# Optimization experiments

Measured on AMD Instinct MI355X. Metric: run time of the kernel, lower is better.

The kernel has to match this reference:

```python
import jax, jax.numpy as jnp
import numpy as np

B, S, H, R, K, L = 8, 2048, 512, 7, 10, 4
OFFSETS = np.array([-3, -2, -1, 1, 2, 3], dtype=np.int32)
BN_EPS = 1e-5


def setup_inputs() -> dict:
    key = jax.random.key(0)
    ks = jax.random.split(key, 12)
    u = lambda k, shape, s: jax.random.uniform(k, shape, minval=-s, maxval=s, dtype=jnp.float32)
    s3, sh, shr = 1.0 / np.sqrt(3.0), 1.0 / np.sqrt(H), 1.0 / np.sqrt(R * H)
    return {
        "n_coords": jax.random.normal(ks[0], (B, S, 3), jnp.float32),
        "ca_coords": jax.random.normal(ks[1], (B, S, 3), jnp.float32),
        "c_coords": jax.random.normal(ks[2], (B, S, 3), jnp.float32),
        "Wp": u(ks[3], (H, 3), s3),
        "bp": u(ks[4], (H,), s3),
        "Wlin": u(ks[5], (L, H, R * H), shr),
        "blin": u(ks[6], (L, H), shr),
        "Wself": u(ks[7], (L, H, H), sh),
        "bself": u(ks[8], (L, H), sh),
        "bn_gamma": jnp.ones((L, H), jnp.float32),
        "bn_beta": jnp.zeros((L, H), jnp.float32),
        "bn_mean": jax.random.normal(ks[9], (L, H), jnp.float32) * 0.1,
        "bn_var": jax.random.uniform(ks[10], (L, H), minval=0.5, maxval=1.5, dtype=jnp.float32),
    }


def _edges(pos):
    """Edge list per graph: sequential offsets -3..3 -> relations 0..5, KNN(k=10) -> relation 6."""
    i = jnp.arange(S)
    off = jnp.asarray(OFFSETS)
    dst_seq = i[:, None] + off[None, :]                            # [S,6]
    valid = (dst_seq >= 0) & (dst_seq < S)
    src_seq = jnp.broadcast_to(i[:, None], (S, 6))
    rel_seq = jnp.broadcast_to(jnp.arange(6, dtype=jnp.int32)[None, :], (S, 6))
    dst_seq = jnp.clip(dst_seq, 0, S - 1)
    # squared distances give the same topk-smallest ordering as torch.norm
    d2 = jnp.sum((pos[:, None, :] - pos[None, :, :]) ** 2, axis=-1)  # [S,S]
    _, knn = jax.lax.top_k(-d2, K + 1)                             # k+1 smallest, self first
    dst_knn = knn[:, 1:]                                           # drop self
    src_knn = jnp.broadcast_to(i[:, None], (S, K))
    rel_knn = jnp.full((S, K), 6, dtype=jnp.int32)
    src = jnp.concatenate([src_seq.reshape(-1), src_knn.reshape(-1)])
    dst = jnp.concatenate([dst_seq.reshape(-1), dst_knn.reshape(-1)])
    rel = jnp.concatenate([rel_seq.reshape(-1), rel_knn.reshape(-1)])
    w = jnp.concatenate([valid.reshape(-1).astype(pos.dtype),
                         jnp.ones((S * K,), pos.dtype)])
    return src, dst, rel, w


def _gearnet(ca_coords, Wp, bp, Wlin, blin, Wself, bself, bn_gamma, bn_beta, bn_mean, bn_var):
    def per_graph(pos):
        src, dst, rel, w = _edges(pos)
        seg = dst * R + rel                                        # node_out*num_relation + relation
        h = pos @ Wp.T + bp                                        # coord_projection: Linear(3, H)
        for l in range(L):
            msg = h[src] * w[:, None]                              # [E,H] gather + edge weight
            upd = jax.ops.segment_sum(msg, seg, num_segments=S * R)  # scatter-add per (node, relation)
            upd = upd.reshape(S, R * H)
            out = upd @ Wlin[l].T + blin[l] + h @ Wself[l].T + bself[l]
            out = (out - bn_mean[l]) * jax.lax.rsqrt(bn_var[l] + BN_EPS) * bn_gamma[l] + bn_beta[l]
            h = jax.nn.relu(out) + h                               # relu then short_cut residual
        return h
    return jax.vmap(per_graph)(ca_coords)                          # [B,S,H]


def reference(n_coords, ca_coords, c_coords, Wp, bp, Wlin, blin, Wself, bself,
              bn_gamma, bn_beta, bn_mean, bn_var):
    # n_coords / c_coords are accepted but unused, exactly as in the original forward.
    return _gearnet(ca_coords, Wp, bp, Wlin, blin, Wself, bself,
                    bn_gamma, bn_beta, bn_mean, bn_var)
```

## Files before the change

### kernel.cpp

```cpp
#include <hip/hip_runtime.h>
#include <stdint.h>

#define B_ 8
#define S_ 2048
#define H_ 512
#define R_ 7
#define K_ 10
#define L_ 4
#define KT_ 4096
#define RH_ 3584

typedef __attribute__((ext_vector_type(8))) short bf16x8;
typedef __attribute__((ext_vector_type(4))) float f32x4;
typedef __attribute__((ext_vector_type(4))) unsigned short u16x4;
typedef unsigned long long u64;

__device__ __forceinline__ unsigned short f2bf(float f){
  unsigned int u = __float_as_uint(f);
  u = (u + 0x7fffu + ((u >> 16) & 1u)) >> 16;
  return (unsigned short)u;
}

__device__ __forceinline__ float bf2f(unsigned short s){
  return __uint_as_float(((unsigned int)s) << 16);
}

__device__ __forceinline__ f32x4 bf4load(const unsigned short* p){
  u16x4 v = *(const u16x4*)p;
  f32x4 o;
#pragma unroll
  for (int e = 0; e < 4; e++) o[e] = bf2f(v[e]);
  return o;
}

__device__ __forceinline__ void gload16(const void* g, void* lds){
  __builtin_amdgcn_global_load_lds(
      (const __attribute__((address_space(1))) unsigned int*)g,
      (__attribute__((address_space(3))) unsigned int*)lds, 16, 0, 0);
}

__global__ __launch_bounds__(256) void knn_kernel(const float* __restrict__ pos,
                                                  int* __restrict__ knn){
  __shared__ float px[S_], py[S_], pz[S_];
  int b = blockIdx.y;
  const float* p = pos + (size_t)b * S_ * 3;
  for (int idx = threadIdx.x; idx < S_; idx += 256){
    px[idx] = p[idx*3+0]; py[idx] = p[idx*3+1]; pz[idx] = p[idx*3+2];
  }
  __syncthreads();
  int w = threadIdx.x >> 6, l = threadIdx.x & 63;
  int i = blockIdx.x * 4 + w;
  float xi = px[i], yi = py[i], zi = pz[i];
  u64 best[10];
#pragma unroll
  for (int q = 0; q < 10; q++) best[q] = ~0ull;
  for (int j = l; j < S_; j += 64){
    if (j == i) continue;
    float dx = __fsub_rn(xi, px[j]);
    float dy = __fsub_rn(yi, py[j]);
    float dz = __fsub_rn(zi, pz[j]);
    float d2 = __fadd_rn(__fadd_rn(__fmul_rn(dx,dx), __fmul_rn(dy,dy)), __fmul_rn(dz,dz));
    u64 key = ((u64)__float_as_uint(d2) << 32) | (unsigned)j;
    if (key < best[9]){
      best[9] = key;
#pragma unroll
      for (int q = 9; q > 0; --q){
        u64 a = best[q-1], c = best[q];
        u64 lo = a < c ? a : c, hi = a < c ? c : a;
        best[q-1] = lo; best[q] = hi;
      }
    }
  }
  int* out = knn + ((size_t)b * S_ + i) * K_;
#pragma unroll
  for (int t = 0; t < 10; t++){
    u64 cand = best[0];
    u64 m = cand;
#pragma unroll
    for (int o = 32; o; o >>= 1){
      u64 other = __shfl_xor(m, o);
      if (other < m) m = other;
    }
    if (cand == m){
#pragma unroll
      for (int q = 0; q < 9; q++) best[q] = best[q+1];
      best[9] = ~0ull;
    }
    if (l == 0) out[t] = (int)(unsigned)(m & 0xffffffffu);
  }
}

__global__ void count_kernel(const int* __restrict__ knn, int* __restrict__ counts){
  int idx = blockIdx.x * 256 + threadIdx.x;
  int b = idx / (S_ * K_);
  int d = knn[idx];
  atomicAdd(&counts[b * S_ + d], 1);
}

__global__ __launch_bounds__(256) void scan_kernel(const int* __restrict__ counts,
                                                   int* __restrict__ row_start,
                                                   int* __restrict__ cursor){
  __shared__ int lds[256];
  int b = blockIdx.x, t = threadIdx.x;
  int base = b * S_;
  int v[8]; int s = 0;
#pragma unroll
  for (int e = 0; e < 8; e++){ v[e] = s; s += counts[base + t*8 + e]; }
  lds[t] = s;
  __syncthreads();
  int total = s;
  for (int o = 1; o < 256; o <<= 1){
    int add = 0;
    if (t >= o) add = lds[t - o];
    __syncthreads();
    lds[t] += add;
    __syncthreads();
  }
  int ex = lds[t] - total;
  int rb = b * (S_ + 1);
#pragma unroll
  for (int e = 0; e < 8; e++){
    int val = ex + v[e];
    row_start[rb + t*8 + e] = val;
    cursor[base + t*8 + e] = val;
  }
  if (t == 255) row_start[rb + S_] = lds[255];
}

__global__ void fill_kernel(const int* __restrict__ knn, int* __restrict__ cursor,
                            int* __restrict__ col){
  int idx = blockIdx.x * 256 + threadIdx.x;
  int b = idx / (S_ * K_);
  int i = (idx / K_) % S_;
  int d = knn[idx];
  int p = atomicAdd(&cursor[b * S_ + d], 1);
  col[(size_t)b * S_ * K_ + p] = i;
}

__global__ void sort_kernel(const int* __restrict__ row_start, int* __restrict__ col){
  int idx = blockIdx.x * 256 + threadIdx.x;
  int b = idx / S_, d = idx % S_;
  int rs = row_start[b*(S_+1)+d], re = row_start[b*(S_+1)+d+1];
  int* c = col + (size_t)b * S_ * K_;
  for (int a = rs + 1; a < re; ++a){
    int vv = c[a]; int q = a - 1;
    while (q >= rs && c[q] > vv){ c[q+1] = c[q]; --q; }
    c[q+1] = vv;
  }
}

__global__ void prepw_kernel(const float* __restrict__ Wlin, const float* __restrict__ Wself,
                             unsigned short* __restrict__ Wt){
  size_t e = ((size_t)blockIdx.x * 256 + threadIdx.x) * 8;
  int k = (int)(e & 4095);
  int j = (int)((e >> 12) & 511);
  int l = (int)(e >> 21);
  const float* src = (k < RH_) ? Wlin + ((size_t)l * H_ + j) * RH_ + k
                               : Wself + ((size_t)l * H_ + j) * H_ + (k - RH_);
  union { unsigned short s[8]; uint4 u; } pk;
#pragma unroll
  for (int t = 0; t < 8; t++) pk.s[t] = f2bf(src[t]);
  *(uint4*)&Wt[e] = pk.u;
}

__global__ void prepa_kernel(const float* __restrict__ gam, const float* __restrict__ bet,
                             const float* __restrict__ mean, const float* __restrict__ var,
                             const float* __restrict__ blin, const float* __restrict__ bself,
                             float* __restrict__ scale, float* __restrict__ shift){
  int idx = blockIdx.x * 256 + threadIdx.x;
  float sc = gam[idx] * rsqrtf(var[idx] + 1e-5f);
  scale[idx] = sc;
  shift[idx] = bet[idx] + (blin[idx] + bself[idx] - mean[idx]) * sc;
}

__global__ void inith_kernel(const float* __restrict__ pos, const float* __restrict__ Wp,
                             const float* __restrict__ bp, float* __restrict__ h,
                             unsigned short* __restrict__ hb){
  int idx = blockIdx.x * 256 + threadIdx.x;
  int j = (idx & 127) * 4;
  int bs = idx >> 7;
  const float* p = pos + (size_t)bs * 3;
  float x = p[0], y = p[1], z = p[2];
  f32x4 o;
#pragma unroll
  for (int e = 0; e < 4; e++){
    const float* wr = Wp + (j + e) * 3;
    o[e] = x * wr[0] + y * wr[1] + z * wr[2] + bp[j + e];
  }
  *(f32x4*)&h[(size_t)bs * H_ + j] = o;
  unsigned int w0 = f2bf(o[0]) | ((unsigned)f2bf(o[1]) << 16);
  unsigned int w1 = f2bf(o[2]) | ((unsigned)f2bf(o[3]) << 16);
  uint2 u; u.x = w0; u.y = w1;
  *(uint2*)&hb[(size_t)bs * H_ + j] = u;
}

__global__ __launch_bounds__(128) void hknn_kernel(const unsigned short* __restrict__ hb,
                                                   const int* __restrict__ row_start,
                                                   const int* __restrict__ col,
                                                   unsigned short* __restrict__ hk){
  int bx = blockIdx.x;
  int d = (bx & 7) * 256 + (bx >> 3);
  int b = blockIdx.y;
  int j = threadIdx.x * 4;
  int rs = row_start[b * (S_ + 1) + d];
  int re = row_start[b * (S_ + 1) + d + 1];
  const int* cl = col + (size_t)b * S_ * K_;
  f32x4 acc = {0.f, 0.f, 0.f, 0.f};
  for (int e = rs; e < re; ++e){
    int i = cl[e];
    acc += bf4load(&hb[((size_t)b * S_ + i) * H_ + j]);
  }
  u16x4 v;
#pragma unroll
  for (int e = 0; e < 4; e++) v[e] = f2bf(acc[e]);
  *(u16x4*)&hk[((size_t)b * S_ + d) * H_ + j] = v;
}

__global__ __launch_bounds__(256) void gemmf_kernel(
    const unsigned short* __restrict__ hbin,
    const unsigned short* __restrict__ hkn,
    const unsigned short* __restrict__ Wt,
    float* __restrict__ h,
    unsigned short* __restrict__ hbout,
    const float* __restrict__ scale,
    const float* __restrict__ shift,
    const unsigned short* __restrict__ zbuf){
  __shared__ unsigned short As[4][128 * 32];
  __shared__ unsigned short Bs[4][128 * 32];
  int tid = threadIdx.x;
  int nwg = gridDim.x;
  int q = nwg >> 3;
  int wg = blockIdx.x;
  int swz = (wg & 7) * q + (wg >> 3);
  int my = swz >> 2;
  int nx = swz & 3;
  int l = tid & 63, w = tid >> 6;
  int wrow = (w >> 1) * 64, wcol = (w & 1) * 64;
  int aBase = my * 128;
  int bBase = nx * 128;
  f32x4 acc[4][4] = {};

  int row0 = tid >> 2;
  int kc = (tid & 3) ^ ((row0 >> 1) & 3);
  int gr0 = aBase + row0, gr1 = gr0 + 64;
  const unsigned short* Bb0 = Wt + (size_t)(bBase + row0) * KT_ + kc * 8;
  const unsigned short* Bb1 = Wt + (size_t)(bBase + row0 + 64) * KT_ + kc * 8;
  int dst0 = tid * 8, dst1 = (tid + 256) * 8;

  const unsigned short *sa0, *sa1, *sb0, *sb1;

#define SETSLICE(rs) do {                                                     \
    int _r = (rs);                                                            \
    const unsigned short *_a0, *_a1;                                          \
    if (_r < 6){                                                              \
      int _sh = (_r < 3) ? (3 - _r) : (2 - _r);          \
      int _s0 = gr0 + _sh, _s1 = gr1 + _sh;                                   \
      _a0 = (((unsigned)_s0 >> 11) == ((unsigned)gr0 >> 11)) ? hbin + (size_t)_s0 * H_ : zbuf; \
      _a1 = (((unsigned)_s1 >> 11) == ((unsigned)gr1 >> 11)) ? hbin + (size_t)_s1 * H_ : zbuf; \
    } else {                                                                  \
      const unsigned short* _bs = (_r == 6) ? hkn : hbin;                     \
      _a0 = _bs + (size_t)gr0 * H_; _a1 = _bs + (size_t)gr1 * H_;             \
    }                                                                         \
    sa0 = _a0 + kc * 8; sa1 = _a1 + kc * 8;                                   \
    sb0 = Bb0 + _r * 512; sb1 = Bb1 + _r * 512;                               \
  } while (0)

#define STAGE(sl, ksl) do { int _ko = (ksl) * 32;          \
    gload16(sa0 + _ko, &As[sl][dst0]);                     \
    gload16(sa1 + _ko, &As[sl][dst1]);                     \
    gload16(sb0 + _ko, &Bs[sl][dst0]);                     \
    gload16(sb1 + _ko, &Bs[sl][dst1]);                     \
  } while (0)

  SETSLICE(0);
  STAGE(0, 0); STAGE(1, 1); STAGE(2, 2);

  int kcr = l >> 4, lr = l & 15;
  int s = 0;
  for (int r = 0; r < 8; ++r){
#pragma unroll
    for (int ks = 0; ks < 16; ++ks){
      int s3 = s + 3; if (s3 >= 4) s3 -= 4;
      if (r < 7 || ks < 13){
        if (ks == 13) SETSLICE(r + 1);
        STAGE(s3, (ks + 3) & 15);
      }
      if (r < 7 || ks < 13)  asm volatile("s_waitcnt vmcnt(12)" ::: "memory");
      else if (ks == 13)     asm volatile("s_waitcnt vmcnt(8)" ::: "memory");
      else if (ks == 14)     asm volatile("s_waitcnt vmcnt(4)" ::: "memory");
      else                   asm volatile("s_waitcnt vmcnt(0)" ::: "memory");
      __builtin_amdgcn_s_barrier();
      asm volatile("" ::: "memory");

      const unsigned short* Abuf = As[s];
      const unsigned short* Bbuf = Bs[s];
      bf16x8 af[4], bf[4];
#pragma unroll
      for (int mi = 0; mi < 4; mi++){
        int row = wrow + mi * 16 + lr;
        int slot = kcr ^ ((row >> 1) & 3);
        af[mi] = *(const bf16x8*)&Abuf[row * 32 + slot * 8];
      }
#pragma unroll
      for (int ni = 0; ni < 4; ni++){
        int row = wcol + ni * 16 + lr;
        int slot = kcr ^ ((row >> 1) & 3);
        bf[ni] = *(const bf16x8*)&Bbuf[row * 32 + slot * 8];
      }
      __builtin_amdgcn_s_setprio(1);
#pragma unroll
      for (int mi = 0; mi < 4; mi++)
#pragma unroll
        for (int ni = 0; ni < 4; ni++)
          acc[mi][ni] = __builtin_amdgcn_mfma_f32_16x16x32_bf16(af[mi], bf[ni], acc[mi][ni], 0, 0, 0);
      __builtin_amdgcn_s_setprio(0);
      asm volatile("" ::: "memory");
      __builtin_amdgcn_s_barrier();
      asm volatile("" ::: "memory");
      ++s; if (s == 4) s = 0;
    }
  }
#undef STAGE
#undef SETSLICE

  int r0 = (l >> 4) * 4, c0 = l & 15;
#pragma unroll
  for (int ni = 0; ni < 4; ni++){
    int gcol = bBase + wcol + ni * 16 + c0;
    float sc = scale[gcol], sf = shift[gcol];
#pragma unroll
    for (int mi = 0; mi < 4; mi++){
#pragma unroll
      for (int reg = 0; reg < 4; reg++){
        int grow = aBase + wrow + mi * 16 + r0 + reg;
        size_t o = (size_t)grow * H_ + gcol;
        float val = fmaxf(acc[mi][ni][reg] * sc + sf, 0.f);
        float hv = h[o] + val;
        h[o] = hv;
        hbout[o] = f2bf(hv);
      }
    }
  }
}

extern "C" void kernel_launch(void* const* d_in, const int* in_sizes, int n_in,
                              void* d_out, int out_size, void* d_ws, size_t ws_size,
                              hipStream_t stream){
  const float* ca    = (const float*)d_in[1];
  const float* Wp    = (const float*)d_in[3];
  const float* bp    = (const float*)d_in[4];
  const float* Wlin  = (const float*)d_in[5];
  const float* blin  = (const float*)d_in[6];
  const float* Wself = (const float*)d_in[7];
  const float* bself = (const float*)d_in[8];
  const float* gam   = (const float*)d_in[9];
  const float* bet   = (const float*)d_in[10];
  const float* mean  = (const float*)d_in[11];
  const float* var   = (const float*)d_in[12];
  float* h = (float*)d_out;

  char* ws = (char*)d_ws;
  size_t off = 0;
  auto alloc = [&](size_t bytes) -> char* {
    char* p = ws + off;
    off = (off + bytes + 255) & ~(size_t)255;
    return p;
  };
  int* knn       = (int*)alloc((size_t)B_ * S_ * K_ * 4);
  int* counts    = (int*)alloc((size_t)B_ * S_ * 4);
  int* row_start = (int*)alloc((size_t)B_ * (S_ + 1) * 4);
  int* cursor    = (int*)alloc((size_t)B_ * S_ * 4);
  int* col       = (int*)alloc((size_t)B_ * S_ * K_ * 4);
  unsigned short* Wt  = (unsigned short*)alloc((size_t)L_ * H_ * KT_ * 2);
  float* scale   = (float*)alloc((size_t)L_ * H_ * 4);
  float* shift   = (float*)alloc((size_t)L_ * H_ * 4);
  unsigned short* hbA = (unsigned short*)alloc((size_t)B_ * S_ * H_ * 2);
  unsigned short* hbB = (unsigned short*)alloc((size_t)B_ * S_ * H_ * 2);
  unsigned short* hkn = (unsigned short*)alloc((size_t)B_ * S_ * H_ * 2);
  unsigned short* zbuf = (unsigned short*)alloc(4096 * 2);

  hipMemsetAsync(counts, 0, (size_t)B_ * S_ * 4, stream);
  hipMemsetAsync(zbuf, 0, 4096 * 2, stream);
  knn_kernel<<<dim3(S_ / 4, B_), 256, 0, stream>>>(ca, knn);
  count_kernel<<<dim3(B_ * S_ * K_ / 256), 256, 0, stream>>>(knn, counts);
  scan_kernel<<<dim3(B_), 256, 0, stream>>>(counts, row_start, cursor);
  fill_kernel<<<dim3(B_ * S_ * K_ / 256), 256, 0, stream>>>(knn, cursor, col);
  sort_kernel<<<dim3(B_ * S_ / 256), 256, 0, stream>>>(row_start, col);
  prepw_kernel<<<dim3((int)((size_t)L_ * H_ * KT_ / 8 / 256)), 256, 0, stream>>>(Wlin, Wself, Wt);
  prepa_kernel<<<dim3(L_ * H_ / 256), 256, 0, stream>>>(gam, bet, mean, var, blin, bself, scale, shift);
  inith_kernel<<<dim3(B_ * S_ * (H_ / 4) / 256), 256, 0, stream>>>(ca, Wp, bp, h, hbA);

  for (int l = 0; l < L_; l++){
    unsigned short* in  = (l & 1) ? hbB : hbA;
    unsigned short* out = (l & 1) ? hbA : hbB;
    hknn_kernel<<<dim3(S_, B_), 128, 0, stream>>>(in, row_start, col, hkn);
    gemmf_kernel<<<dim3((B_ * S_ / 128) * 4), 256, 0, stream>>>(
        in, hkn, Wt + (size_t)l * H_ * KT_, h, out,
        scale + l * H_, shift + l * H_, zbuf);
  }
}
```

Baseline: 600.7 us.

## Shrink GEMM M-tile to 64 rows with 3-stage pipeline; pack kNN coords as float4

The fused GEMM tile is cut from 128x128 to 64x128, so each warp holds a 32x64 sub-tile, and the LDS pipeline is reduced from 4 stages to 3 with adjusted vmcnt waits. This halves the LDS and accumulator footprint and doubles the number of workgroups (1024 vs 512), aiming for better occupancy and CU fill on the 256-CU part. The cost is less reuse of the B tile per A load, which means more weight traffic, plus a shallower prefetch depth. Separately, the kNN kernel stores coordinates as float4 in LDS so each neighbor needs one vector load instead of three scalar loads.

```diff
diff --git a/kernel.cpp b/kernel.cpp
--- a/kernel.cpp
+++ b/kernel.cpp
@@ -41,24 +41,27 @@
 
 __global__ __launch_bounds__(256) void knn_kernel(const float* __restrict__ pos,
                                                   int* __restrict__ knn){
-  __shared__ float px[S_], py[S_], pz[S_];
+  __shared__ float4 p4[S_];
   int b = blockIdx.y;
   const float* p = pos + (size_t)b * S_ * 3;
   for (int idx = threadIdx.x; idx < S_; idx += 256){
-    px[idx] = p[idx*3+0]; py[idx] = p[idx*3+1]; pz[idx] = p[idx*3+2];
+    float4 v; v.x = p[idx*3+0]; v.y = p[idx*3+1]; v.z = p[idx*3+2]; v.w = 0.f;
+    p4[idx] = v;
   }
   __syncthreads();
   int w = threadIdx.x >> 6, l = threadIdx.x & 63;
   int i = blockIdx.x * 4 + w;
-  float xi = px[i], yi = py[i], zi = pz[i];
+  float4 pi = p4[i];
+  float xi = pi.x, yi = pi.y, zi = pi.z;
   u64 best[10];
 #pragma unroll
   for (int q = 0; q < 10; q++) best[q] = ~0ull;
   for (int j = l; j < S_; j += 64){
     if (j == i) continue;
-    float dx = __fsub_rn(xi, px[j]);
-    float dy = __fsub_rn(yi, py[j]);
-    float dz = __fsub_rn(zi, pz[j]);
+    float4 pj = p4[j];
+    float dx = __fsub_rn(xi, pj.x);
+    float dy = __fsub_rn(yi, pj.y);
+    float dz = __fsub_rn(zi, pj.z);
     float d2 = __fadd_rn(__fadd_rn(__fmul_rn(dx,dx), __fmul_rn(dy,dy)), __fmul_rn(dz,dz));
     u64 key = ((u64)__float_as_uint(d2) << 32) | (unsigned)j;
     if (key < best[9]){
@@ -225,8 +228,8 @@
     const float* __restrict__ scale,
     const float* __restrict__ shift,
     const unsigned short* __restrict__ zbuf){
-  __shared__ unsigned short As[4][128 * 32];
-  __shared__ unsigned short Bs[4][128 * 32];
+  __shared__ unsigned short As[3][64 * 32];
+  __shared__ unsigned short Bs[3][128 * 32];
   int tid = threadIdx.x;
   int nwg = gridDim.x;
   int q = nwg >> 3;
@@ -235,68 +238,68 @@
   int my = swz >> 2;
   int nx = swz & 3;
   int l = tid & 63, w = tid >> 6;
-  int wrow = (w >> 1) * 64, wcol = (w & 1) * 64;
-  int aBase = my * 128;
+  int wrow = (w >> 1) * 32, wcol = (w & 1) * 64;
+  int aBase = my * 64;
   int bBase = nx * 128;
-  f32x4 acc[4][4] = {};
-
-  int row0 = tid >> 2;
-  int kc = (tid & 3) ^ ((row0 >> 1) & 3);
-  int gr0 = aBase + row0, gr1 = gr0 + 64;
-  const unsigned short* Bb0 = Wt + (size_t)(bBase + row0) * KT_ + kc * 8;
-  const unsigned short* Bb1 = Wt + (size_t)(bBase + row0 + 64) * KT_ + kc * 8;
-  int dst0 = tid * 8, dst1 = (tid + 256) * 8;
-
-  const unsigned short *sa0, *sa1, *sb0, *sb1;
+  f32x4 acc[2][4] = {};
+
+  int rowA = tid >> 2;
+  int kcA = (tid & 3) ^ ((rowA >> 1) & 3);
+  int gr0 = aBase + rowA;
+  int rb0 = tid >> 2, rb1 = rb0 + 64;
+  int kcB0 = (tid & 3) ^ ((rb0 >> 1) & 3);
+  int kcB1 = (tid & 3) ^ ((rb1 >> 1) & 3);
+  const unsigned short* Bb0 = Wt + (size_t)(bBase + rb0) * KT_ + kcB0 * 8;
+  const unsigned short* Bb1 = Wt + (size_t)(bBase + rb1) * KT_ + kcB1 * 8;
+  int dstA = tid * 8, dstB0 = tid * 8, dstB1 = (tid + 256) * 8;
+
+  const unsigned short *sa0, *sb0, *sb1;
 
 #define SETSLICE(rs) do {                                                     \
     int _r = (rs);                                                            \
-    const unsigned short *_a0, *_a1;                                          \
+    const unsigned short *_a0;                                                \
     if (_r < 6){                                                              \
       int _sh = (_r < 3) ? (3 - _r) : (2 - _r);          \
-      int _s0 = gr0 + _sh, _s1 = gr1 + _sh;                                   \
+      int _s0 = gr0 + _sh;                                                    \
       _a0 = (((unsigned)_s0 >> 11) == ((unsigned)gr0 >> 11)) ? hbin + (size_t)_s0 * H_ : zbuf; \
-      _a1 = (((unsigned)_s1 >> 11) == ((unsigned)gr1 >> 11)) ? hbin + (size_t)_s1 * H_ : zbuf; \
     } else {                                                                  \
       const unsigned short* _bs = (_r == 6) ? hkn : hbin;                     \
-      _a0 = _bs + (size_t)gr0 * H_; _a1 = _bs + (size_t)gr1 * H_;             \
+      _a0 = _bs + (size_t)gr0 * H_;                                           \
     }                                                                         \
-    sa0 = _a0 + kc * 8; sa1 = _a1 + kc * 8;                                   \
+    sa0 = _a0 + kcA * 8;                                                      \
     sb0 = Bb0 + _r * 512; sb1 = Bb1 + _r * 512;                               \
   } while (0)
 
 #define STAGE(sl, ksl) do { int _ko = (ksl) * 32;          \
-    gload16(sa0 + _ko, &As[sl][dst0]);                     \
-    gload16(sa1 + _ko, &As[sl][dst1]);                     \
-    gload16(sb0 + _ko, &Bs[sl][dst0]);                     \
-    gload16(sb1 + _ko, &Bs[sl][dst1]);                     \
+    gload16(sa0 + _ko, &As[sl][dstA]);                     \
+    gload16(sb0 + _ko, &Bs[sl][dstB0]);                    \
+    gload16(sb1 + _ko, &Bs[sl][dstB1]);                    \
   } while (0)
 
   SETSLICE(0);
-  STAGE(0, 0); STAGE(1, 1); STAGE(2, 2);
+  STAGE(0, 0); STAGE(1, 1);
 
   int kcr = l >> 4, lr = l & 15;
   int s = 0;
   for (int r = 0; r < 8; ++r){
 #pragma unroll
     for (int ks = 0; ks < 16; ++ks){
-      int s3 = s + 3; if (s3 >= 4) s3 -= 4;
-      if (r < 7 || ks < 13){
-        if (ks == 13) SETSLICE(r + 1);
-        STAGE(s3, (ks + 3) & 15);
+      int s2 = s + 2; if (s2 >= 3) s2 -= 3;
+      if (r < 7 || ks < 14){
+        if (ks == 14) SETSLICE(r + 1);
+        STAGE(s2, (ks + 2) & 15);
       }
-      if (r < 7 || ks < 13)  asm volatile("s_waitcnt vmcnt(12)" ::: "memory");
-      else if (ks == 13)     asm volatile("s_waitcnt vmcnt(8)" ::: "memory");
-      else if (ks == 14)     asm volatile("s_waitcnt vmcnt(4)" ::: "memory");
-      else                   asm volatile("s_waitcnt vmcnt(0)" ::: "memory");
+      if (r < 7 || ks < 14)       asm volatile("s_waitcnt vmcnt(6)" ::: "memory");
+      else if (ks == 14)          asm volatile("s_waitcnt vmcnt(3)" ::: "memory");
+      else                        asm volatile("s_waitcnt vmcnt(0)" ::: "memory");
       __builtin_amdgcn_s_barrier();
       asm volatile("" ::: "memory");
 
       const unsigned short* Abuf = As[s];
       const unsigned short* Bbuf = Bs[s];
-      bf16x8 af[4], bf[4];
-#pragma unroll
-      for (int mi = 0; mi < 4; mi++){
+      bf16x8 af[2], bf[4];
+#pragma unroll
+      for (int mi = 0; mi < 2; mi++){
         int row = wrow + mi * 16 + lr;
         int slot = kcr ^ ((row >> 1) & 3);
         af[mi] = *(const bf16x8*)&Abuf[row * 32 + slot * 8];
@@ -309,7 +312,7 @@
       }
       __builtin_amdgcn_s_setprio(1);
 #pragma unroll
-      for (int mi = 0; mi < 4; mi++)
+      for (int mi = 0; mi < 2; mi++)
 #pragma unroll
         for (int ni = 0; ni < 4; ni++)
           acc[mi][ni] = __builtin_amdgcn_mfma_f32_16x16x32_bf16(af[mi], bf[ni], acc[mi][ni], 0, 0, 0);
@@ -317,7 +320,7 @@
       asm volatile("" ::: "memory");
       __builtin_amdgcn_s_barrier();
       asm volatile("" ::: "memory");
-      ++s; if (s == 4) s = 0;
+      ++s; if (s == 3) s = 0;
     }
   }
 #undef STAGE
@@ -329,7 +332,7 @@
     int gcol = bBase + wcol + ni * 16 + c0;
     float sc = scale[gcol], sf = shift[gcol];
 #pragma unroll
-    for (int mi = 0; mi < 4; mi++){
+    for (int mi = 0; mi < 2; mi++){
 #pragma unroll
       for (int reg = 0; reg < 4; reg++){
         int grow = aBase + wrow + mi * 16 + r0 + reg;
@@ -394,7 +397,7 @@
     unsigned short* in  = (l & 1) ? hbB : hbA;
     unsigned short* out = (l & 1) ? hbA : hbB;
     hknn_kernel<<<dim3(S_, B_), 128, 0, stream>>>(in, row_start, col, hkn);
-    gemmf_kernel<<<dim3((B_ * S_ / 128) * 4), 256, 0, stream>>>(
+    gemmf_kernel<<<dim3((B_ * S_ / 64) * 4), 256, 0, stream>>>(
         in, hkn, Wt + (size_t)l * H_ * KT_, h, out,
         scale + l * H_, shift + l * H_, zbuf);
   }
```

After: 673.1 us. 1.12x slower.
